# Performance work log

Measured on AMD Instinct MI355X. Metric: run time of the kernel, lower is better.

Reference implementation:

```python
import jax, jax.numpy as jnp
import numpy as np

B, V, T, K, N = 2048, 256, 11, 8, 8
H = 2 ** N - 1  # 255 combination neurons per slot


def setup_inputs() -> dict:
    key = jax.random.key(0)
    k0, k1, k2, k3, k4 = jax.random.split(key, 5)
    # one-hot character ids, matching make_scanner_batch semantics: (B, V, T, K)
    ids = jax.random.randint(k0, (B, T, K), 0, V)
    x_unfolded = jax.nn.one_hot(ids, V, axis=1, dtype=jnp.float32)
    # scanner_w ~ U(-1/sqrt(V), 1/sqrt(V)), shape (N, V, K)
    bv = 1.0 / np.sqrt(V).astype(np.float32)
    scanner_w = jax.random.uniform(k1, (N, V, K), jnp.float32, -bv, bv)
    # grouped 1x1 conv: torch weight (K*H, N, 1) -> store (K*H, N); fan_in = N
    bh = 1.0 / np.sqrt(N).astype(np.float32)
    hidden_w = jax.random.uniform(k2, (K * H, N), jnp.float32, -bh, bh)
    # output 1x1 conv: (2, K*H, 1) -> (2, K*H); fan_in = K*H
    bo = 1.0 / np.sqrt(K * H).astype(np.float32)
    out_w = jax.random.uniform(k3, (2, K * H), jnp.float32, -bo, bo)
    out_b = jax.random.uniform(k4, (2,), jnp.float32, -bo, bo)
    return {"x_unfolded": x_unfolded, "scanner_w": scanner_w,
            "hidden_w": hidden_w, "out_w": out_w, "out_b": out_b}


def reference(x_unfolded, scanner_w, hidden_w, out_w, out_b):
    # x_unfolded: (B, V, T, K); scanner_w: (N, V, K)
    b, v, t, k = x_unfolded.shape
    n = scanner_w.shape[0]
    h_per_slot = hidden_w.shape[0] // k
    # one-hot matmul (equivalent to a gather): result (B, K, N, T),
    # i.e. channel order after reshape is slot-major (k*N + n), matching
    # torch's permute(0,3,1,2).reshape(B, K*N, T).
    h = jax.nn.relu(jnp.einsum('bvtk,nvk->bknt', x_unfolded, scanner_w))
    # grouped 1x1 conv with groups=K: group k maps its N scanner values to
    # h_per_slot neurons. torch weight (K*H, N, 1) -> (K, H, N), where output
    # channel o belongs to group o // H.
    hw = hidden_w.reshape(k, h_per_slot, n)
    h2 = jax.nn.relu(jnp.einsum('bknt,khn->bkht', h, hw)).reshape(b, k * h_per_slot, t)
    # final 1x1 conv with bias: (B, 2, T)
    return jnp.einsum('bct,oc->bot', h2, out_w) + out_b[None, :, None]
```

## Files before the change

### kernel.cpp

```cpp
#include <hip/hip_runtime.h>

constexpr int B_ = 2048;
constexpr int V_ = 256;
constexpr int T_ = 11;
constexpr int K_ = 8;
constexpr int N_ = 8;
constexpr int H_ = 255;
constexpr int TK = T_ * K_;
constexpr int XB = V_ * TK;
constexpr int SLAB = 92;

__global__ __launch_bounds__(256)
void prep_srw(const float* __restrict__ sw, float* __restrict__ srw) {
    const int i = blockIdx.x * 256 + threadIdx.x;
    if (i < V_ * K_ * N_) {
        const int n  = i & 7;
        const int vk = i >> 3;
        const int k  = vk & 7;
        const int v  = vk >> 3;
        srw[i] = fmaxf(sw[(n * V_ + v) * K_ + k], 0.0f);
    }
}

__global__ __launch_bounds__(256, 3)
void scanner_fused(const float* __restrict__ x,
                   const float* __restrict__ srw,
                   const float* __restrict__ hw,
                   const float* __restrict__ ow,
                   const float* __restrict__ ob,
                   float* __restrict__ out)
{
    __shared__ int   ids_sh[TK];
    __shared__ float hsh[K_ * SLAB];
    __shared__ float wred[4][22];

    const int tid = threadIdx.x;
    const int b   = blockIdx.x;

    const float4* xb = (const float4*)(x + (size_t)b * XB);
    #pragma unroll
    for (int c = 0; c < 3; ++c) {
        const int nload = (c < 2) ? 8 : 6;
        float4 vbuf[8];
        #pragma unroll
        for (int i = 0; i < 8; ++i)
            if (i < nload) vbuf[i] = xb[(c * 8 + i) * 256 + tid];
        #pragma unroll
        for (int i = 0; i < 8; ++i) {
            if (i < nload) {
                const float4 q = vbuf[i];
                if ((q.x + q.y) + (q.z + q.w) != 0.0f) {
                    const int F = ((c * 8 + i) * 256 + tid) * 4;
                    if (q.x != 0.0f) { const int f = F;     const int v = f / TK; ids_sh[f - v * TK] = v; }
                    if (q.y != 0.0f) { const int f = F + 1; const int v = f / TK; ids_sh[f - v * TK] = v; }
                    if (q.z != 0.0f) { const int f = F + 2; const int v = f / TK; ids_sh[f - v * TK] = v; }
                    if (q.w != 0.0f) { const int f = F + 3; const int v = f / TK; ids_sh[f - v * TK] = v; }
                }
            }
        }
    }
    __syncthreads();

    if (tid < TK) {
        const int v = ids_sh[tid];
        const int t = tid >> 3;
        const int k = tid & 7;
        const float4* p = (const float4*)(srw + (v * K_ + k) * N_);
        const float4 a0 = p[0];
        const float4 a1 = p[1];
        float4* d = (float4*)(hsh + k * SLAB + t * 8);
        d[0] = a0;
        d[1] = a1;
    }
    __syncthreads();

    const int k2 = tid >> 5;
    const int hb = tid & 31;

    float hreg[T_][N_];
    #pragma unroll
    for (int t = 0; t < T_; ++t) {
        const float4* p = (const float4*)(hsh + k2 * SLAB + t * 8);
        const float4 a0 = p[0];
        const float4 a1 = p[1];
        hreg[t][0] = a0.x; hreg[t][1] = a0.y; hreg[t][2] = a0.z; hreg[t][3] = a0.w;
        hreg[t][4] = a1.x; hreg[t][5] = a1.y; hreg[t][6] = a1.z; hreg[t][7] = a1.w;
    }

    float acc0[T_], acc1[T_];
    #pragma unroll
    for (int t = 0; t < T_; ++t) { acc0[t] = 0.0f; acc1[t] = 0.0f; }

    #pragma unroll
    for (int i = 0; i < 8; ++i) {
        const int hh = hb + 32 * i;
        if (hh < H_) {
            const int row = k2 * H_ + hh;
            const float4* hwp = (const float4*)(hw + row * 8);
            const float4 w0 = hwp[0];
            const float4 w1 = hwp[1];
            const float o0 = ow[row];
            const float o1 = ow[K_ * H_ + row];
            #pragma unroll
            for (int t = 0; t < T_; ++t) {
                float pre = w0.x * hreg[t][0];
                pre = fmaf(w0.y, hreg[t][1], pre);
                pre = fmaf(w0.z, hreg[t][2], pre);
                pre = fmaf(w0.w, hreg[t][3], pre);
                pre = fmaf(w1.x, hreg[t][4], pre);
                pre = fmaf(w1.y, hreg[t][5], pre);
                pre = fmaf(w1.z, hreg[t][6], pre);
                pre = fmaf(w1.w, hreg[t][7], pre);
                const float h2 = fmaxf(pre, 0.0f);
                acc0[t] = fmaf(h2, o0, acc0[t]);
                acc1[t] = fmaf(h2, o1, acc1[t]);
            }
        }
    }

    #pragma unroll
    for (int t = 0; t < T_; ++t) {
        #pragma unroll
        for (int off = 32; off >= 1; off >>= 1) {
            acc0[t] += __shfl_xor(acc0[t], off, 64);
            acc1[t] += __shfl_xor(acc1[t], off, 64);
        }
    }
    const int wave = tid >> 6;
    const int lane = tid & 63;
    if (lane == 0) {
        #pragma unroll
        for (int t = 0; t < T_; ++t) {
            wred[wave][t]      = acc0[t];
            wred[wave][11 + t] = acc1[t];
        }
    }
    __syncthreads();

    if (tid < 22) {
        const float s = wred[0][tid] + wred[1][tid] + wred[2][tid] + wred[3][tid];
        out[(size_t)b * 22 + tid] = s + ob[tid / 11];
    }
}

extern "C" void kernel_launch(void* const* d_in, const int* in_sizes, int n_in,
                              void* d_out, int out_size, void* d_ws, size_t ws_size,
                              hipStream_t stream) {
    const float* x  = (const float*)d_in[0];
    const float* sw = (const float*)d_in[1];
    const float* hw = (const float*)d_in[2];
    const float* ow = (const float*)d_in[3];
    const float* ob = (const float*)d_in[4];
    float* out = (float*)d_out;

    float* srw = (float*)d_ws;

    prep_srw<<<(V_ * K_ * N_ + 255) / 256, 256, 0, stream>>>(sw, srw);
    scanner_fused<<<B_, 256, 0, stream>>>(x, srw, hw, ow, ob, out);
}
```

Baseline: 271.9 us.

## Fold scanner relu into main kernel and split time loop to cut registers

Removes the separate prep kernel and has the 88 gather threads read scanner weights directly with a strided per-n gather and relu. Splits the T loop into two halves so only 6x8 hidden values stay live in registers, and raises the launch-bounds occupancy hint from 3 to 4 blocks per SIMD. This trades one kernel launch and some register pressure for reloading the hidden-weight rows twice and doing uncoalesced scanner-weight loads. The inner t loops lack unroll pragmas, so with runtime indices acc[] may spill to scratch.

```diff
diff --git a/kernel.cpp b/kernel.cpp
--- a/kernel.cpp
+++ b/kernel.cpp
@@ -10,21 +10,9 @@
 constexpr int XB = V_ * TK;
 constexpr int SLAB = 92;
 
-__global__ __launch_bounds__(256)
-void prep_srw(const float* __restrict__ sw, float* __restrict__ srw) {
-    const int i = blockIdx.x * 256 + threadIdx.x;
-    if (i < V_ * K_ * N_) {
-        const int n  = i & 7;
-        const int vk = i >> 3;
-        const int k  = vk & 7;
-        const int v  = vk >> 3;
-        srw[i] = fmaxf(sw[(n * V_ + v) * K_ + k], 0.0f);
-    }
-}
-
-__global__ __launch_bounds__(256, 3)
+__global__ __launch_bounds__(256, 4)
 void scanner_fused(const float* __restrict__ x,
-                   const float* __restrict__ srw,
+                   const float* __restrict__ sw,
                    const float* __restrict__ hw,
                    const float* __restrict__ ow,
                    const float* __restrict__ ob,
@@ -65,55 +53,59 @@
         const int v = ids_sh[tid];
         const int t = tid >> 3;
         const int k = tid & 7;
-        const float4* p = (const float4*)(srw + (v * K_ + k) * N_);
-        const float4 a0 = p[0];
-        const float4 a1 = p[1];
-        float4* d = (float4*)(hsh + k * SLAB + t * 8);
-        d[0] = a0;
-        d[1] = a1;
+        float* d = hsh + k * SLAB + t * 8;
+        #pragma unroll
+        for (int n = 0; n < N_; ++n)
+            d[n] = fmaxf(sw[(n * V_ + v) * K_ + k], 0.0f);
     }
     __syncthreads();
 
     const int k2 = tid >> 5;
     const int hb = tid & 31;
 
-    float hreg[T_][N_];
-    #pragma unroll
-    for (int t = 0; t < T_; ++t) {
-        const float4* p = (const float4*)(hsh + k2 * SLAB + t * 8);
-        const float4 a0 = p[0];
-        const float4 a1 = p[1];
-        hreg[t][0] = a0.x; hreg[t][1] = a0.y; hreg[t][2] = a0.z; hreg[t][3] = a0.w;
-        hreg[t][4] = a1.x; hreg[t][5] = a1.y; hreg[t][6] = a1.z; hreg[t][7] = a1.w;
-    }
-
     float acc0[T_], acc1[T_];
     #pragma unroll
     for (int t = 0; t < T_; ++t) { acc0[t] = 0.0f; acc1[t] = 0.0f; }
 
     #pragma unroll
-    for (int i = 0; i < 8; ++i) {
-        const int hh = hb + 32 * i;
-        if (hh < H_) {
-            const int row = k2 * H_ + hh;
-            const float4* hwp = (const float4*)(hw + row * 8);
-            const float4 w0 = hwp[0];
-            const float4 w1 = hwp[1];
-            const float o0 = ow[row];
-            const float o1 = ow[K_ * H_ + row];
-            #pragma unroll
-            for (int t = 0; t < T_; ++t) {
-                float pre = w0.x * hreg[t][0];
-                pre = fmaf(w0.y, hreg[t][1], pre);
-                pre = fmaf(w0.z, hreg[t][2], pre);
-                pre = fmaf(w0.w, hreg[t][3], pre);
-                pre = fmaf(w1.x, hreg[t][4], pre);
-                pre = fmaf(w1.y, hreg[t][5], pre);
-                pre = fmaf(w1.z, hreg[t][6], pre);
-                pre = fmaf(w1.w, hreg[t][7], pre);
-                const float h2 = fmaxf(pre, 0.0f);
-                acc0[t] = fmaf(h2, o0, acc0[t]);
-                acc1[t] = fmaf(h2, o1, acc1[t]);
+    for (int half = 0; half < 2; ++half) {
+        const int t0 = (half == 0) ? 0 : 6;
+        const int t1 = (half == 0) ? 6 : T_;
+
+        float hreg[6][N_];
+        for (int t = t0; t < t1; ++t) {
+            const float4* p = (const float4*)(hsh + k2 * SLAB + t * 8);
+            const float4 a0 = p[0];
+            const float4 a1 = p[1];
+            float* hr = hreg[t - t0];
+            hr[0] = a0.x; hr[1] = a0.y; hr[2] = a0.z; hr[3] = a0.w;
+            hr[4] = a1.x; hr[5] = a1.y; hr[6] = a1.z; hr[7] = a1.w;
+        }
+
+        #pragma unroll
+        for (int i = 0; i < 8; ++i) {
+            const int hh = hb + 32 * i;
+            if (hh < H_) {
+                const int row = k2 * H_ + hh;
+                const float4* hwp = (const float4*)(hw + row * 8);
+                const float4 w0 = hwp[0];
+                const float4 w1 = hwp[1];
+                const float o0 = ow[row];
+                const float o1 = ow[K_ * H_ + row];
+                for (int t = t0; t < t1; ++t) {
+                    const float* hr = hreg[t - t0];
+                    float pre = w0.x * hr[0];
+                    pre = fmaf(w0.y, hr[1], pre);
+                    pre = fmaf(w0.z, hr[2], pre);
+                    pre = fmaf(w0.w, hr[3], pre);
+                    pre = fmaf(w1.x, hr[4], pre);
+                    pre = fmaf(w1.y, hr[5], pre);
+                    pre = fmaf(w1.z, hr[6], pre);
+                    pre = fmaf(w1.w, hr[7], pre);
+                    const float h2 = fmaxf(pre, 0.0f);
+                    acc0[t] = fmaf(h2, o0, acc0[t]);
+                    acc1[t] = fmaf(h2, o1, acc1[t]);
+                }
             }
         }
     }
@@ -153,8 +145,5 @@
     const float* ob = (const float*)d_in[4];
     float* out = (float*)d_out;
 
-    float* srw = (float*)d_ws;
-
-    prep_srw<<<(V_ * K_ * N_ + 255) / 256, 256, 0, stream>>>(sw, srw);
-    scanner_fused<<<B_, 256, 0, stream>>>(x, srw, hw, ow, ob, out);
+    scanner_fused<<<B_, 256, 0, stream>>>(x, sw, hw, ow, ob, out);
 }
```

Result: slower. 283.1 us (+4.1%).
